# Optimization experiments

Hardware: AMD Instinct MI355X
Metric: run time of the kernel (lower is better)

The kernel has to match this reference:

```python
import jax, jax.numpy as jnp
import numpy as np


def setup_inputs() -> dict:
    key = jax.random.key(0)
    k1, k2, k3 = jax.random.split(key, 3)
    bs, r, d = 4, 4096, 64
    G = jax.random.uniform(k1, (bs, d), dtype=jnp.float32)          # eigenvalues (non-negative)
    V = jax.random.normal(k2, (bs, r, d), dtype=jnp.float32)        # eigenvectors / spectral embedding
    weights = jax.random.uniform(k3, (1,), dtype=jnp.float32)       # learned scalar t
    return {"G": G, "V": V, "weights": weights}


def reference(G, V, weights):
    # Original: eVs = diag(max(G,0)^(2t)); y = E@eVs@Phi2^T + Phi2@eVs@E^T - 2*Phi@eVs@Phi^T
    # Since eVs is diagonal, this is the weighted pairwise squared distance:
    # y[b,i,j] = sum_k w[b,k] * (V[b,i,k] - V[b,j,k])^2 with w = max(G,0)^(2t).
    t = weights[0]
    w = jnp.maximum(G, jnp.zeros_like(G)) ** (2.0 * t)   # (bs, d)
    Vw = V * w[:, None, :]                               # (bs, r, d) elementwise diag scaling
    s = jnp.sum(Vw * V, axis=-1)                         # (bs, r): weighted squared norms
    cross = jnp.einsum('brd,bsd->brs', Vw, V)            # (bs, r, r)
    y = s[:, :, None] + s[:, None, :] - 2.0 * cross
    return y
```

## Files before the change

### kernel.cpp

```cpp
#include <hip/hip_runtime.h>
#include <hip/hip_bf16.h>


typedef __attribute__((ext_vector_type(8))) short bf16x8;
typedef __attribute__((ext_vector_type(4))) float f32x4;

constexpr int BS = 4, R = 4096, D = 64;
constexpr int LS = 260;

__device__ __forceinline__ void barrier_lds_only() {
    asm volatile("s_waitcnt lgkmcnt(0)" ::: "memory");
    __builtin_amdgcn_sched_barrier(0);
    __builtin_amdgcn_s_barrier();
    __builtin_amdgcn_sched_barrier(0);
}

__global__ __launch_bounds__(256) void prep_kernel(
    const float* __restrict__ G, const float* __restrict__ V,
    const float* __restrict__ wt,
    __hip_bfloat16* __restrict__ u_bf, float* __restrict__ s)
{
    int row  = blockIdx.x * 4 + (threadIdx.x >> 6);
    int lane = threadIdx.x & 63;
    if (row >= BS * R) return;
    int b = row / R;

    float t  = wt[0];
    float g  = fmaxf(G[b * D + lane], 0.0f);
    float sw = powf(g, t);
    float u  = sw * V[(size_t)row * D + lane];

    __hip_bfloat16 ub = __float2bfloat16(u);
    u_bf[(size_t)row * D + lane] = ub;

    float uf   = __bfloat162float(ub);
    float prod = uf * uf;
    #pragma unroll
    for (int off = 32; off; off >>= 1) prod += __shfl_down(prod, off);
    if (lane == 0) s[row] = prod;
}

__global__ __launch_bounds__(512) void dist_kernel(
    const short* __restrict__ U, const float* __restrict__ s,
    float* __restrict__ out)
{
    __shared__ float lds[64 * LS];

    int lane = threadIdx.x & 63;
    int wave = threadIdx.x >> 6;
    int wr   = wave >> 2;
    int wc   = wave & 3;

    int b  = blockIdx.z;
    int jb = blockIdx.x * 256;
    int i0 = blockIdx.y * 128;

    const short* Ap = U + ((size_t)b * R + i0 + wr * 64) * D;
    const short* Bp = U + ((size_t)b * R + jb + wc * 64) * D;
    const float* sb = s + (size_t)b * R;

    int lrow = lane & 15;
    int kgrp = lane >> 4;

    bf16x8 a[4][2];
    #pragma unroll
    for (int rb = 0; rb < 4; ++rb)
        #pragma unroll
        for (int ks = 0; ks < 2; ++ks)
            a[rb][ks] = *(const bf16x8*)(Ap + (rb * 16 + lrow) * D + ks * 32 + kgrp * 8);

    f32x4 acc[4][4];
    #pragma unroll
    for (int rb = 0; rb < 4; ++rb)
        #pragma unroll
        for (int jt = 0; jt < 4; ++jt)
            acc[rb][jt] = f32x4{0.f, 0.f, 0.f, 0.f};

    #pragma unroll
    for (int jt = 0; jt < 4; ++jt) {
        const short* Bt = Bp + jt * 16 * D;
        bf16x8 b0 = *(const bf16x8*)(Bt + lrow * D +      kgrp * 8);
        bf16x8 b1 = *(const bf16x8*)(Bt + lrow * D + 32 + kgrp * 8);
        #pragma unroll
        for (int rb = 0; rb < 4; ++rb) {
            acc[rb][jt] = __builtin_amdgcn_mfma_f32_16x16x32_bf16(a[rb][0], b0, acc[rb][jt], 0, 0, 0);
            acc[rb][jt] = __builtin_amdgcn_mfma_f32_16x16x32_bf16(a[rb][1], b1, acc[rb][jt], 0, 0, 0);
        }
    }

    float si_lane = sb[i0 + wr * 64 + lane];

    float* outb = out + ((size_t)b * R + i0) * R + jb;

    #pragma unroll
    for (int c = 0; c < 2; ++c) {
        if (wr == c) {
            #pragma unroll
            for (int rb = 0; rb < 4; ++rb) {
                #pragma unroll
                for (int rg = 0; rg < 4; ++rg) {
                    int rl = rb * 16 + kgrp * 4 + rg;
                    float si = __shfl(si_lane, rl);
                    #pragma unroll
                    for (int jt = 0; jt < 4; ++jt) {
                        float sj = sb[jb + wc * 64 + jt * 16 + lrow];
                        float y  = si + sj - 2.0f * acc[rb][jt][rg];
                        lds[rl * LS + wc * 64 + jt * 16 + lrow] = y;
                    }
                }
            }
        }
        barrier_lds_only();

        #pragma unroll
        for (int r = 0; r < 8; ++r) {
            int rl = wave * 8 + r;
            f32x4 v = *(const f32x4*)&lds[rl * LS + lane * 4];
            *(f32x4*)(outb + (size_t)(c * 64 + rl) * R + lane * 4) = v;
        }
        if (c == 0) barrier_lds_only();
    }
}

extern "C" void kernel_launch(void* const* d_in, const int* in_sizes, int n_in,
                              void* d_out, int out_size, void* d_ws, size_t ws_size,
                              hipStream_t stream) {
    const float* G  = (const float*)d_in[0];
    const float* V  = (const float*)d_in[1];
    const float* wt = (const float*)d_in[2];
    float* out = (float*)d_out;

    char* ws = (char*)d_ws;
    __hip_bfloat16* u_bf = (__hip_bfloat16*)ws;
    float*          s    = (float*)        (ws + (size_t)BS * R * D * 2);

    prep_kernel<<<BS * R / 4, 256, 0, stream>>>(G, V, wt, u_bf, s);

    dim3 grid(R / 256, R / 128, BS);
    dist_kernel<<<grid, 512, 0, stream>>>((const short*)u_bf, s, out);
}
```

Before: 64.77 us.

## Fuse weight scaling and bf16 conversion into distance kernel, shrink prep to tiny kernel

```diff
diff --git a/kernel.cpp b/kernel.cpp
--- a/kernel.cpp
+++ b/kernel.cpp
@@ -15,33 +15,21 @@
     __builtin_amdgcn_sched_barrier(0);
 }
 
-__global__ __launch_bounds__(256) void prep_kernel(
-    const float* __restrict__ G, const float* __restrict__ V,
-    const float* __restrict__ wt,
-    __hip_bfloat16* __restrict__ u_bf, float* __restrict__ s)
+__global__ __launch_bounds__(256) void sw_kernel(
+    const float* __restrict__ G, const float* __restrict__ wt,
+    float* __restrict__ sw)
 {
-    int row  = blockIdx.x * 4 + (threadIdx.x >> 6);
-    int lane = threadIdx.x & 63;
-    if (row >= BS * R) return;
-    int b = row / R;
-
-    float t  = wt[0];
-    float g  = fmaxf(G[b * D + lane], 0.0f);
-    float sw = powf(g, t);
-    float u  = sw * V[(size_t)row * D + lane];
-
-    __hip_bfloat16 ub = __float2bfloat16(u);
-    u_bf[(size_t)row * D + lane] = ub;
-
-    float uf   = __bfloat162float(ub);
-    float prod = uf * uf;
-    #pragma unroll
-    for (int off = 32; off; off >>= 1) prod += __shfl_down(prod, off);
-    if (lane == 0) s[row] = prod;
+    int i = threadIdx.x;
+    float t = wt[0];
+    float g = fmaxf(G[i], 0.0f);
+    float r;
+    if (g > 0.0f) r = __powf(g, t);
+    else          r = (t == 0.0f) ? 1.0f : 0.0f;
+    sw[i] = r;
 }
 
-__global__ __launch_bounds__(512) void dist_kernel(
-    const short* __restrict__ U, const float* __restrict__ s,
+__global__ __launch_bounds__(512, 4) void dist_kernel(
+    const float* __restrict__ V, const float* __restrict__ sw,
     float* __restrict__ out)
 {
     __shared__ float lds[64 * LS];
@@ -55,19 +43,52 @@
     int jb = blockIdx.x * 256;
     int i0 = blockIdx.y * 128;
 
-    const short* Ap = U + ((size_t)b * R + i0 + wr * 64) * D;
-    const short* Bp = U + ((size_t)b * R + jb + wc * 64) * D;
-    const float* sb = s + (size_t)b * R;
-
     int lrow = lane & 15;
     int kgrp = lane >> 4;
 
+    const float* Vb  = V + (size_t)b * R * D;
+    const float* swb = sw + b * D;
+
+    f32x4 sw0a = *(const f32x4*)(swb +      kgrp * 8);
+    f32x4 sw0b = *(const f32x4*)(swb +      kgrp * 8 + 4);
+    f32x4 sw1a = *(const f32x4*)(swb + 32 + kgrp * 8);
+    f32x4 sw1b = *(const f32x4*)(swb + 32 + kgrp * 8 + 4);
+
+    auto cvt8 = [](const float* vp, const f32x4& wa, const f32x4& wb, float& p) {
+        f32x4 v0 = *(const f32x4*)vp;
+        f32x4 v1 = *(const f32x4*)(vp + 4);
+        bf16x8 r;
+        #pragma unroll
+        for (int i = 0; i < 4; ++i) {
+            __hip_bfloat16 h = __float2bfloat16(wa[i] * v0[i]);
+            unsigned short bits; __builtin_memcpy(&bits, &h, 2);
+            r[i] = (short)bits;
+            float uf = __bfloat162float(h);
+            p = fmaf(uf, uf, p);
+        }
+        #pragma unroll
+        for (int i = 0; i < 4; ++i) {
+            __hip_bfloat16 h = __float2bfloat16(wb[i] * v1[i]);
+            unsigned short bits; __builtin_memcpy(&bits, &h, 2);
+            r[4 + i] = (short)bits;
+            float uf = __bfloat162float(h);
+            p = fmaf(uf, uf, p);
+        }
+        return r;
+    };
+
     bf16x8 a[4][2];
+    float si_lane = 0.0f;
     #pragma unroll
-    for (int rb = 0; rb < 4; ++rb)
-        #pragma unroll
-        for (int ks = 0; ks < 2; ++ks)
-            a[rb][ks] = *(const bf16x8*)(Ap + (rb * 16 + lrow) * D + ks * 32 + kgrp * 8);
+    for (int rb = 0; rb < 4; ++rb) {
+        const float* vp = Vb + (size_t)(i0 + wr * 64 + rb * 16 + lrow) * D + kgrp * 8;
+        float p = 0.0f;
+        a[rb][0] = cvt8(vp,      sw0a, sw0b, p);
+        a[rb][1] = cvt8(vp + 32, sw1a, sw1b, p);
+        p += __shfl_xor(p, 16);
+        p += __shfl_xor(p, 32);
+        if (kgrp == rb) si_lane = p;
+    }
 
     f32x4 acc[4][4];
     #pragma unroll
@@ -76,19 +97,22 @@
         for (int jt = 0; jt < 4; ++jt)
             acc[rb][jt] = f32x4{0.f, 0.f, 0.f, 0.f};
 
+    float sB[4];
     #pragma unroll
     for (int jt = 0; jt < 4; ++jt) {
-        const short* Bt = Bp + jt * 16 * D;
-        bf16x8 b0 = *(const bf16x8*)(Bt + lrow * D +      kgrp * 8);
-        bf16x8 b1 = *(const bf16x8*)(Bt + lrow * D + 32 + kgrp * 8);
+        const float* vp = Vb + (size_t)(jb + wc * 64 + jt * 16 + lrow) * D + kgrp * 8;
+        float p = 0.0f;
+        bf16x8 b0 = cvt8(vp,      sw0a, sw0b, p);
+        bf16x8 b1 = cvt8(vp + 32, sw1a, sw1b, p);
+        p += __shfl_xor(p, 16);
+        p += __shfl_xor(p, 32);
+        sB[jt] = p;
         #pragma unroll
         for (int rb = 0; rb < 4; ++rb) {
             acc[rb][jt] = __builtin_amdgcn_mfma_f32_16x16x32_bf16(a[rb][0], b0, acc[rb][jt], 0, 0, 0);
             acc[rb][jt] = __builtin_amdgcn_mfma_f32_16x16x32_bf16(a[rb][1], b1, acc[rb][jt], 0, 0, 0);
         }
     }
-
-    float si_lane = sb[i0 + wr * 64 + lane];
 
     float* outb = out + ((size_t)b * R + i0) * R + jb;
 
@@ -103,8 +127,7 @@
                     float si = __shfl(si_lane, rl);
                     #pragma unroll
                     for (int jt = 0; jt < 4; ++jt) {
-                        float sj = sb[jb + wc * 64 + jt * 16 + lrow];
-                        float y  = si + sj - 2.0f * acc[rb][jt][rg];
+                        float y  = si + sB[jt] - 2.0f * acc[rb][jt][rg];
                         lds[rl * LS + wc * 64 + jt * 16 + lrow] = y;
                     }
                 }
@@ -130,12 +153,10 @@
     const float* wt = (const float*)d_in[2];
     float* out = (float*)d_out;
 
-    char* ws = (char*)d_ws;
-    __hip_bfloat16* u_bf = (__hip_bfloat16*)ws;
-    float*          s    = (float*)        (ws + (size_t)BS * R * D * 2);
+    float* swbuf = (float*)d_ws;
 
-    prep_kernel<<<BS * R / 4, 256, 0, stream>>>(G, V, wt, u_bf, s);
+    sw_kernel<<<1, 256, 0, stream>>>(G, wt, swbuf);
 
     dim3 grid(R / 256, R / 128, BS);
-    dist_kernel<<<grid, 512, 0, stream>>>((const short*)u_bf, s, out);
+    dist_kernel<<<grid, 512, 0, stream>>>(V, swbuf, out);
 }
```

Result: slower. 89.32 us (+37.9%).
